# Performance work log

Hardware: AMD Instinct MI355X
Metric: run time of the kernel (lower is better)

## Reference

```python
import jax, jax.numpy as jnp
import numpy as np

MIN_NORM = 1e-15
BALL_EPS = 4e-3  # fp32 boundary eps used by PoincareBall.proj


def _artanh(x):
    x = jnp.clip(x, -1.0 + 1e-7, 1.0 - 1e-7)
    return 0.5 * (jnp.log1p(x) - jnp.log1p(-x))


def _norm(x):
    return jnp.maximum(jnp.linalg.norm(x, axis=-1, keepdims=True), MIN_NORM)


def mobius_matvec(m, x, c):
    sqrt_c = jnp.sqrt(c)
    x_norm = _norm(x)
    mx = x @ m  # [N, out]
    mx_norm = _norm(mx)
    res_c = jnp.tanh(mx_norm / x_norm * _artanh(sqrt_c * x_norm)) * mx / (mx_norm * sqrt_c)
    cond = jnp.all(mx == 0, axis=-1, keepdims=True)
    return jnp.where(cond, jnp.zeros((), dtype=x.dtype), res_c)


def expmap0(u, c):
    sqrt_c = jnp.sqrt(c)
    u_norm = _norm(u)
    return jnp.tanh(sqrt_c * u_norm) * u / (sqrt_c * u_norm)


def logmap0(p, c):
    sqrt_c = jnp.sqrt(c)
    p_norm = _norm(p)
    return _artanh(sqrt_c * p_norm) * p / (sqrt_c * p_norm)


def proj(x, c):
    norm = _norm(x)
    maxnorm = (1.0 - BALL_EPS) / jnp.sqrt(c)
    return jnp.where(norm > maxnorm, x / norm * maxnorm, x)


def mobius_add(x, y, c):
    x2 = jnp.sum(x * x, axis=-1, keepdims=True)
    y2 = jnp.sum(y * y, axis=-1, keepdims=True)
    xy = jnp.sum(x * y, axis=-1, keepdims=True)
    num = (1.0 + 2.0 * c * xy + c * y2) * x + (1.0 - c * x2) * y
    denom = 1.0 + 2.0 * c * xy + c * c * x2 * y2
    return num / jnp.maximum(denom, MIN_NORM)


def setup_inputs() -> dict:
    key = jax.random.key(0)
    N, E, IN, OUT = 50000, 800000, 256, 64
    ks = jax.random.split(key, 6)
    x = jax.random.normal(ks[0], (N, IN), dtype=jnp.float32) * 0.1
    weight = jax.random.normal(ks[1], (IN, OUT), dtype=jnp.float32) / np.sqrt(IN)
    bias = jax.random.normal(ks[2], (OUT,), dtype=jnp.float32) * 0.01
    vals = jax.random.uniform(ks[3], (E,), dtype=jnp.float32) / 16.0  # ~normalized adj
    row = jax.random.randint(ks[4], (E,), 0, N, dtype=jnp.int32)
    col = jax.random.randint(ks[5], (E,), 0, N, dtype=jnp.int32)
    c = jnp.asarray(1.0, dtype=jnp.float32)
    return {"x": x, "weight": weight, "bias": bias, "vals": vals, "c": c, "row": row, "col": col}


def reference(x, weight, bias, vals, c, row, col):
    N = x.shape[0]
    out = mobius_matvec(weight, x, c)
    # proj_tan0 is identity on the Poincare ball
    hyp_bias = proj(expmap0(bias[None, :], c), c)
    out = mobius_add(out, hyp_bias, c)
    out = logmap0(out, c)
    # sparse.mm(adj, out): gather neighbor rows, weight by edge vals, scatter-add
    out = jax.ops.segment_sum(vals[:, None] * out[col], row, num_segments=N)
    out = proj(expmap0(out, c), c)
    return out
```

## Files before the change

kernel.cpp:

```cpp
#include <hip/hip_runtime.h>
#include <math.h>

#define MIN_NORM 1e-15f
#define BALL_EPS 4e-3f

typedef __attribute__((ext_vector_type(8))) short bf16x8;
typedef __attribute__((ext_vector_type(4))) float f32x4;

__device__ __forceinline__ short f2bf(float f) {
  unsigned u = __builtin_bit_cast(unsigned, f);
  u = u + 0x7FFFu + ((u >> 16) & 1u);
  return (short)(u >> 16);
}
__device__ __forceinline__ float bf2f(unsigned short us) {
  unsigned u = ((unsigned)us) << 16;
  return __builtin_bit_cast(float, u);
}

__device__ __forceinline__ float wsum(float v) {
#pragma unroll
  for (int off = 32; off; off >>= 1) v += __shfl_xor(v, off, 64);
  return v;
}

__device__ __forceinline__ float artanh_clip(float z) {
  z = fminf(fmaxf(z, -1.0f + 1e-7f), 1.0f - 1e-7f);
  return 0.5f * (log1pf(z) - log1pf(-z));
}

__global__ __launch_bounds__(256) void k1_hyp_hist(
    const float* __restrict__ x, const float* __restrict__ W,
    const float* __restrict__ bias, const float* __restrict__ cptr,
    unsigned short* __restrict__ h, int N,
    const int* __restrict__ row, int* __restrict__ cnt, int E, int G1) {
  if ((int)blockIdx.x >= G1) {
    const int nb = gridDim.x - G1;
    for (int i = (blockIdx.x - G1) * 256 + threadIdx.x; i < E; i += nb * 256)
      atomicAdd(&cnt[row[i]], 1);
    return;
  }
  const int lane = threadIdx.x & 63;
  const int wid = threadIdx.x >> 6;
  const int m = lane & 15;
  const int g = lane >> 4;
  const float c = *cptr;
  const float sc = sqrtf(c);
  const float maxnorm = (1.0f - BALL_EPS) / sc;

  bf16x8 b[8][4];
#pragma unroll
  for (int kk = 0; kk < 8; ++kk)
#pragma unroll
    for (int t = 0; t < 4; ++t) {
      const float* wp = &W[(kk * 32 + g * 8) * 64 + t * 16 + m];
      bf16x8 bb;
#pragma unroll
      for (int j = 0; j < 8; ++j) bb[j] = f2bf(wp[j * 64]);
      b[kk][t] = bb;
    }

  float bv[4], bsq = 0.f;
#pragma unroll
  for (int t = 0; t < 4; ++t) { bv[t] = bias[t * 16 + m]; bsq += bv[t] * bv[t]; }
#pragma unroll
  for (int o = 1; o < 16; o <<= 1) bsq += __shfl_xor(bsq, o, 64);
  float bnorm = fmaxf(sqrtf(bsq), MIN_NORM);
  float tb = tanhf(sc * bnorm);
  float bfac = tb / (sc * bnorm);
  float hbn = fmaxf(tb / sc, MIN_NORM);
  float pfac = (hbn > maxnorm) ? (maxnorm / hbn) : 1.0f;
  float hbv[4], y2 = 0.f;
#pragma unroll
  for (int t = 0; t < 4; ++t) { hbv[t] = bv[t] * bfac * pfac; y2 += hbv[t] * hbv[t]; }
#pragma unroll
  for (int o = 1; o < 16; o <<= 1) y2 += __shfl_xor(y2, o, 64);

  const int nb16 = (N + 15) >> 4;
  const int wstep = G1 * 4;
  for (int rb = blockIdx.x * 4 + wid; rb < nb16; rb += wstep) {
    int arow = rb * 16 + m;
    if (arow >= N) arow = N - 1;
    const float* xp = &x[(size_t)arow * 256 + g * 8];

    bf16x8 a[8];
    float x2p = 0.f;
#pragma unroll
    for (int kk = 0; kk < 8; ++kk) {
      float4 v0 = *(const float4*)(xp + kk * 32);
      float4 v1 = *(const float4*)(xp + kk * 32 + 4);
      x2p += v0.x * v0.x + v0.y * v0.y + v0.z * v0.z + v0.w * v0.w +
             v1.x * v1.x + v1.y * v1.y + v1.z * v1.z + v1.w * v1.w;
      bf16x8 aa;
      aa[0] = f2bf(v0.x); aa[1] = f2bf(v0.y); aa[2] = f2bf(v0.z); aa[3] = f2bf(v0.w);
      aa[4] = f2bf(v1.x); aa[5] = f2bf(v1.y); aa[6] = f2bf(v1.z); aa[7] = f2bf(v1.w);
      a[kk] = aa;
    }
    float x2f = x2p;
    x2f += __shfl_xor(x2f, 16, 64);
    x2f += __shfl_xor(x2f, 32, 64);

    f32x4 acc[4];
#pragma unroll
    for (int t = 0; t < 4; ++t) { acc[t][0] = 0.f; acc[t][1] = 0.f; acc[t][2] = 0.f; acc[t][3] = 0.f; }
#pragma unroll
    for (int kk = 0; kk < 8; ++kk)
#pragma unroll
      for (int t = 0; t < 4; ++t)
        acc[t] = __builtin_amdgcn_mfma_f32_16x16x32_bf16(a[kk], b[kk][t], acc[t], 0, 0, 0);

    float x2r[4];
#pragma unroll
    for (int j = 0; j < 4; ++j) x2r[j] = __shfl(x2f, g * 4 + j, 64);

#pragma unroll
    for (int j = 0; j < 4; ++j) {
      float m0 = acc[0][j], m1 = acc[1][j], m2 = acc[2][j], m3 = acc[3][j];
      float msq = m0 * m0 + m1 * m1 + m2 * m2 + m3 * m3;
      int z = (m0 == 0.f) && (m1 == 0.f) && (m2 == 0.f) && (m3 == 0.f);
#pragma unroll
      for (int o = 1; o < 16; o <<= 1) {
        msq += __shfl_xor(msq, o, 64);
        z &= __shfl_xor(z, o, 64);
      }
      float mx_norm = fmaxf(sqrtf(msq), MIN_NORM);
      float x_norm = fmaxf(sqrtf(x2r[j]), MIN_NORM);
      float art = artanh_clip(sc * x_norm);
      float tt = tanhf(mx_norm / x_norm * art);
      float fac = z ? 0.f : (tt / (mx_norm * sc));
      float r0 = m0 * fac, r1 = m1 * fac, r2 = m2 * fac, r3 = m3 * fac;

      float x2m = r0 * r0 + r1 * r1 + r2 * r2 + r3 * r3;
      float xy = r0 * hbv[0] + r1 * hbv[1] + r2 * hbv[2] + r3 * hbv[3];
#pragma unroll
      for (int o = 1; o < 16; o <<= 1) {
        x2m += __shfl_xor(x2m, o, 64);
        xy += __shfl_xor(xy, o, 64);
      }
      float k2 = 1.f + 2.f * c * xy;
      float ca = k2 + c * y2;
      float cb = 1.f - c * x2m;
      float inv = 1.f / fmaxf(k2 + c * c * x2m * y2, MIN_NORM);
      float a0 = (ca * r0 + cb * hbv[0]) * inv;
      float a1 = (ca * r1 + cb * hbv[1]) * inv;
      float a2 = (ca * r2 + cb * hbv[2]) * inv;
      float a3 = (ca * r3 + cb * hbv[3]) * inv;

      float psq = a0 * a0 + a1 * a1 + a2 * a2 + a3 * a3;
#pragma unroll
      for (int o = 1; o < 16; o <<= 1) psq += __shfl_xor(psq, o, 64);
      float p_norm = fmaxf(sqrtf(psq), MIN_NORM);
      float art2 = artanh_clip(sc * p_norm);
      float fac2 = art2 / (sc * p_norm);

      int orow = rb * 16 + g * 4 + j;
      if (orow < N) {
        unsigned short* hp = &h[(size_t)orow * 64 + m];
        hp[0]  = (unsigned short)f2bf(a0 * fac2);
        hp[16] = (unsigned short)f2bf(a1 * fac2);
        hp[32] = (unsigned short)f2bf(a2 * fac2);
        hp[48] = (unsigned short)f2bf(a3 * fac2);
      }
    }
  }
}

__global__ __launch_bounds__(1024) void scan_a(const int* __restrict__ cnt,
                                               int* __restrict__ rowptr,
                                               int* __restrict__ blksum, int N) {
  __shared__ int wsums[16];
  int gid = blockIdx.x * 1024 + threadIdx.x;
  int lane = threadIdx.x & 63, w = threadIdx.x >> 6;
  int v = (gid < N) ? cnt[gid] : 0;
  int s = v;
#pragma unroll
  for (int d = 1; d < 64; d <<= 1) { int t = __shfl_up(s, d, 64); if (lane >= d) s += t; }
  if (lane == 63) wsums[w] = s;
  __syncthreads();
  if (w == 0 && lane < 16) {
    int ss = wsums[lane];
#pragma unroll
    for (int d = 1; d < 16; d <<= 1) { int u = __shfl_up(ss, d, 64); if (lane >= d) ss += u; }
    wsums[lane] = ss;
  }
  __syncthreads();
  if (w > 0) s += wsums[w - 1];
  if (gid < N) rowptr[1 + gid] = s;
  if (threadIdx.x == 1023) blksum[blockIdx.x] = s;
}

__global__ __launch_bounds__(1024) void scan_c(int* __restrict__ rowptr,
                                               const int* __restrict__ blksum,
                                               int N, int nblk) {
  __shared__ int s_off;
  if (threadIdx.x < 64) {
    int acc = 0;
    for (int bidx = threadIdx.x; bidx < (int)blockIdx.x; bidx += 64) acc += blksum[bidx];
#pragma unroll
    for (int off = 32; off; off >>= 1) acc += __shfl_xor(acc, off, 64);
    if (threadIdx.x == 0) s_off = acc;
  }
  __syncthreads();
  int gid = blockIdx.x * 1024 + threadIdx.x;
  if (gid == 0) rowptr[0] = 0;
  if (gid < N) rowptr[1 + gid] += s_off;
}

__global__ __launch_bounds__(256) void scatter_kernel(
    const int* __restrict__ row, const int* __restrict__ col,
    const float* __restrict__ vals, int* __restrict__ rowptr,
    int2* __restrict__ pairs, int E) {
  int i = blockIdx.x * blockDim.x + threadIdx.x;
  if (i < E) {
    int r = row[i];
    int pos = atomicAdd(&rowptr[r], 1);
    pairs[pos] = make_int2(col[i], __builtin_bit_cast(int, vals[i]));
  }
}

__global__ __launch_bounds__(256) void segsum_kernel(
    const unsigned short* __restrict__ h, const int* __restrict__ rowptr,
    const int2* __restrict__ pairs, const float* __restrict__ cptr,
    float* __restrict__ out, int N) {
  const int lane = threadIdx.x & 63;
  const int wid = threadIdx.x >> 6;
  const int sw = lane >> 4;
  const int q = lane & 15;
  int r = blockIdx.x * 4 + wid;
  if (r >= N) return;
  const float c = *cptr;
  const float sc = sqrtf(c);
  const float maxnorm = (1.0f - BALL_EPS) / sc;
  int st = (r > 0) ? rowptr[r - 1] : 0;
  int en = rowptr[r];
  st = __builtin_amdgcn_readfirstlane(st);
  en = __builtin_amdgcn_readfirstlane(en);

  float a0 = 0.f, a1 = 0.f, a2 = 0.f, a3 = 0.f;
#pragma unroll 2
  for (int i = st + sw; i < en; i += 4) {
    int2 pv = pairs[i];
    float vv = __builtin_bit_cast(float, pv.y);
    ushort4 hv = *(const ushort4*)&h[(size_t)pv.x * 64 + q * 4];
    a0 = fmaf(vv, bf2f(hv.x), a0);
    a1 = fmaf(vv, bf2f(hv.y), a1);
    a2 = fmaf(vv, bf2f(hv.z), a2);
    a3 = fmaf(vv, bf2f(hv.w), a3);
  }
  a0 += __shfl_xor(a0, 32, 64); a1 += __shfl_xor(a1, 32, 64);
  a2 += __shfl_xor(a2, 32, 64); a3 += __shfl_xor(a3, 32, 64);
  a0 += __shfl_xor(a0, 16, 64); a1 += __shfl_xor(a1, 16, 64);
  a2 += __shfl_xor(a2, 16, 64); a3 += __shfl_xor(a3, 16, 64);

  float sq = a0 * a0 + a1 * a1 + a2 * a2 + a3 * a3;
#pragma unroll
  for (int o = 1; o < 16; o <<= 1) sq += __shfl_xor(sq, o, 64);
  float un = fmaxf(sqrtf(sq), MIN_NORM);
  float th = tanhf(sc * un);
  float fac = th / (sc * un);
  float p0 = a0 * fac, p1 = a1 * fac, p2 = a2 * fac, p3 = a3 * fac;
  float psq = p0 * p0 + p1 * p1 + p2 * p2 + p3 * p3;
#pragma unroll
  for (int o = 1; o < 16; o <<= 1) psq += __shfl_xor(psq, o, 64);
  float pn = fmaxf(sqrtf(psq), MIN_NORM);
  if (pn > maxnorm) {
    float pf = maxnorm / pn;
    p0 *= pf; p1 *= pf; p2 *= pf; p3 *= pf;
  }
  if (sw == 0)
    *(float4*)&out[(size_t)r * 64 + q * 4] = make_float4(p0, p1, p2, p3);
}

__global__ __launch_bounds__(256) void edge_kernel(
    const unsigned short* __restrict__ h, const float* __restrict__ vals,
    const int* __restrict__ row, const int* __restrict__ col,
    float* __restrict__ out, int E) {
  const int lane = threadIdx.x & 63;
  const int wid0 = (blockIdx.x * blockDim.x + threadIdx.x) >> 6;
  const int nw = (gridDim.x * blockDim.x) >> 6;
  for (int e = wid0; e < E; e += nw) {
    int eu = __builtin_amdgcn_readfirstlane(e);
    float v = vals[eu];
    int r = row[eu];
    int cl = col[eu];
    atomicAdd(&out[(size_t)r * 64 + lane], v * bf2f(h[(size_t)cl * 64 + lane]));
  }
}

__global__ __launch_bounds__(256) void final_kernel(
    float* __restrict__ out, const float* __restrict__ cptr, int N) {
  const int lane = threadIdx.x & 63;
  const int wid0 = (blockIdx.x * blockDim.x + threadIdx.x) >> 6;
  const int nw = (gridDim.x * blockDim.x) >> 6;
  const float c = *cptr;
  const float sc = sqrtf(c);
  const float maxnorm = (1.0f - BALL_EPS) / sc;
  for (int r = wid0; r < N; r += nw) {
    float u = out[(size_t)r * 64 + lane];
    float un = fmaxf(sqrtf(wsum(u * u)), MIN_NORM);
    float th = tanhf(sc * un);
    float p = th * u / (sc * un);
    float pn = fmaxf(sqrtf(wsum(p * p)), MIN_NORM);
    if (pn > maxnorm) p = p / pn * maxnorm;
    out[(size_t)r * 64 + lane] = p;
  }
}

static inline size_t align256(size_t x) { return (x + 255) & ~(size_t)255; }

extern "C" void kernel_launch(void* const* d_in, const int* in_sizes, int n_in,
                              void* d_out, int out_size, void* d_ws, size_t ws_size,
                              hipStream_t stream) {
  const float* x = (const float*)d_in[0];
  const float* W = (const float*)d_in[1];
  const float* bias = (const float*)d_in[2];
  const float* vals = (const float*)d_in[3];
  const float* cptr = (const float*)d_in[4];
  const int* row = (const int*)d_in[5];
  const int* col = (const int*)d_in[6];
  float* out = (float*)d_out;

  const int OUT = in_sizes[2];
  const int IN = in_sizes[1] / OUT;
  const int N = in_sizes[0] / IN;
  const int E = in_sizes[3];

  char* ws = (char*)d_ws;
  size_t o_h = 0;
  size_t o_rowptr = align256(o_h + (size_t)N * 64 * 2);
  size_t o_blk = align256(o_rowptr + (size_t)(N + 1) * 4);
  size_t o_cnt = align256(o_blk + 1024 * 4);
  size_t o_pairs = align256(o_cnt + (size_t)N * 4);
  size_t needed = o_pairs + (size_t)E * 8;

  unsigned short* h = (unsigned short*)(ws + o_h);

  const int nb16 = (N + 15) / 16;
  const int G1 = (nb16 + 7) / 8;

  if (needed <= ws_size) {
    int* rowptr = (int*)(ws + o_rowptr);
    int* blksum = (int*)(ws + o_blk);
    int* cnt = (int*)(ws + o_cnt);
    int2* pairs = (int2*)(ws + o_pairs);

    const int nblk = (N + 1023) / 1024;
    const int eb = (E + 255) / 256;
    const int HB = 256;

    hipMemsetAsync(cnt, 0, (size_t)N * 4, stream);
    k1_hyp_hist<<<G1 + HB, 256, 0, stream>>>(x, W, bias, cptr, h, N, row, cnt, E, G1);
    scan_a<<<nblk, 1024, 0, stream>>>(cnt, rowptr, blksum, N);
    scan_c<<<nblk, 1024, 0, stream>>>(rowptr, blksum, N, nblk);
    scatter_kernel<<<eb, 256, 0, stream>>>(row, col, vals, rowptr, pairs, E);
    segsum_kernel<<<(N + 3) / 4, 256, 0, stream>>>(h, rowptr, pairs, cptr, out, N);
  } else {
    k1_hyp_hist<<<G1, 256, 0, stream>>>(x, W, bias, cptr, h, N, row, (int*)nullptr, 0, G1);
    hipMemsetAsync(d_out, 0, (size_t)out_size * sizeof(float), stream);
    edge_kernel<<<2048, 256, 0, stream>>>(h, vals, row, col, out, E);
    final_kernel<<<1024, 256, 0, stream>>>(out, cptr, N);
  }
}
```

Before: 228.6 us.

## Split GEMM and hyperbolic epilogue into separate kernels via fp32 workspace

Unfuses the first kernel. The MFMA GEMM now writes raw fp32 mx rows and per-row squared norms to workspace, and a new lightweight kernel reads them back with vectorized float4 loads to apply the mobius/logmap epilogue and write bf16 h. The aim is to shorten the GEMM kernel's critical path, lower its register pressure, and give coalesced ushort4 stores instead of strided 2-byte stores. The cost is an extra launch and an extra round trip of N*64*4 bytes through memory. The mx buffer is reused to hold the CSR pairs, which adds a size condition on the fast path.

```diff
diff --git a/kernel.cpp b/kernel.cpp
--- a/kernel.cpp
+++ b/kernel.cpp
@@ -28,10 +28,9 @@
   return 0.5f * (log1pf(z) - log1pf(-z));
 }
 
-__global__ __launch_bounds__(256) void k1_hyp_hist(
+__global__ __launch_bounds__(256) void k1_gemm_hist(
     const float* __restrict__ x, const float* __restrict__ W,
-    const float* __restrict__ bias, const float* __restrict__ cptr,
-    unsigned short* __restrict__ h, int N,
+    float* __restrict__ mx_ws, float* __restrict__ x2_ws, int N,
     const int* __restrict__ row, int* __restrict__ cnt, int E, int G1) {
   if ((int)blockIdx.x >= G1) {
     const int nb = gridDim.x - G1;
@@ -43,9 +42,6 @@
   const int wid = threadIdx.x >> 6;
   const int m = lane & 15;
   const int g = lane >> 4;
-  const float c = *cptr;
-  const float sc = sqrtf(c);
-  const float maxnorm = (1.0f - BALL_EPS) / sc;
 
   bf16x8 b[8][4];
 #pragma unroll
@@ -58,22 +54,6 @@
       for (int j = 0; j < 8; ++j) bb[j] = f2bf(wp[j * 64]);
       b[kk][t] = bb;
     }
-
-  float bv[4], bsq = 0.f;
-#pragma unroll
-  for (int t = 0; t < 4; ++t) { bv[t] = bias[t * 16 + m]; bsq += bv[t] * bv[t]; }
-#pragma unroll
-  for (int o = 1; o < 16; o <<= 1) bsq += __shfl_xor(bsq, o, 64);
-  float bnorm = fmaxf(sqrtf(bsq), MIN_NORM);
-  float tb = tanhf(sc * bnorm);
-  float bfac = tb / (sc * bnorm);
-  float hbn = fmaxf(tb / sc, MIN_NORM);
-  float pfac = (hbn > maxnorm) ? (maxnorm / hbn) : 1.0f;
-  float hbv[4], y2 = 0.f;
-#pragma unroll
-  for (int t = 0; t < 4; ++t) { hbv[t] = bv[t] * bfac * pfac; y2 += hbv[t] * hbv[t]; }
-#pragma unroll
-  for (int o = 1; o < 16; o <<= 1) y2 += __shfl_xor(y2, o, 64);
 
   const int nb16 = (N + 15) >> 4;
   const int wstep = G1 * 4;
@@ -108,60 +88,95 @@
       for (int t = 0; t < 4; ++t)
         acc[t] = __builtin_amdgcn_mfma_f32_16x16x32_bf16(a[kk], b[kk][t], acc[t], 0, 0, 0);
 
-    float x2r[4];
-#pragma unroll
-    for (int j = 0; j < 4; ++j) x2r[j] = __shfl(x2f, g * 4 + j, 64);
-
 #pragma unroll
     for (int j = 0; j < 4; ++j) {
-      float m0 = acc[0][j], m1 = acc[1][j], m2 = acc[2][j], m3 = acc[3][j];
-      float msq = m0 * m0 + m1 * m1 + m2 * m2 + m3 * m3;
-      int z = (m0 == 0.f) && (m1 == 0.f) && (m2 == 0.f) && (m3 == 0.f);
-#pragma unroll
-      for (int o = 1; o < 16; o <<= 1) {
-        msq += __shfl_xor(msq, o, 64);
-        z &= __shfl_xor(z, o, 64);
-      }
-      float mx_norm = fmaxf(sqrtf(msq), MIN_NORM);
-      float x_norm = fmaxf(sqrtf(x2r[j]), MIN_NORM);
-      float art = artanh_clip(sc * x_norm);
-      float tt = tanhf(mx_norm / x_norm * art);
-      float fac = z ? 0.f : (tt / (mx_norm * sc));
-      float r0 = m0 * fac, r1 = m1 * fac, r2 = m2 * fac, r3 = m3 * fac;
-
-      float x2m = r0 * r0 + r1 * r1 + r2 * r2 + r3 * r3;
-      float xy = r0 * hbv[0] + r1 * hbv[1] + r2 * hbv[2] + r3 * hbv[3];
-#pragma unroll
-      for (int o = 1; o < 16; o <<= 1) {
-        x2m += __shfl_xor(x2m, o, 64);
-        xy += __shfl_xor(xy, o, 64);
-      }
-      float k2 = 1.f + 2.f * c * xy;
-      float ca = k2 + c * y2;
-      float cb = 1.f - c * x2m;
-      float inv = 1.f / fmaxf(k2 + c * c * x2m * y2, MIN_NORM);
-      float a0 = (ca * r0 + cb * hbv[0]) * inv;
-      float a1 = (ca * r1 + cb * hbv[1]) * inv;
-      float a2 = (ca * r2 + cb * hbv[2]) * inv;
-      float a3 = (ca * r3 + cb * hbv[3]) * inv;
-
-      float psq = a0 * a0 + a1 * a1 + a2 * a2 + a3 * a3;
-#pragma unroll
-      for (int o = 1; o < 16; o <<= 1) psq += __shfl_xor(psq, o, 64);
-      float p_norm = fmaxf(sqrtf(psq), MIN_NORM);
-      float art2 = artanh_clip(sc * p_norm);
-      float fac2 = art2 / (sc * p_norm);
-
       int orow = rb * 16 + g * 4 + j;
       if (orow < N) {
-        unsigned short* hp = &h[(size_t)orow * 64 + m];
-        hp[0]  = (unsigned short)f2bf(a0 * fac2);
-        hp[16] = (unsigned short)f2bf(a1 * fac2);
-        hp[32] = (unsigned short)f2bf(a2 * fac2);
-        hp[48] = (unsigned short)f2bf(a3 * fac2);
+        float* mp = &mx_ws[(size_t)orow * 64 + m];
+#pragma unroll
+        for (int t = 0; t < 4; ++t) mp[t * 16] = acc[t][j];
       }
     }
-  }
+    if (g == 0 && rb * 16 + m < N) x2_ws[rb * 16 + m] = x2f;
+  }
+}
+
+__global__ __launch_bounds__(256) void k1b_hyp(
+    const float* __restrict__ mx_ws, const float* __restrict__ x2_ws,
+    const float* __restrict__ bias, const float* __restrict__ cptr,
+    unsigned short* __restrict__ h, int N) {
+  const int lane = threadIdx.x & 63;
+  const int wid = threadIdx.x >> 6;
+  const int sub = lane >> 4;
+  const int q = lane & 15;
+  const float c = *cptr;
+  const float sc = sqrtf(c);
+  const float maxnorm = (1.0f - BALL_EPS) / sc;
+
+  float4 bv = *(const float4*)&bias[q * 4];
+  float bsq = bv.x * bv.x + bv.y * bv.y + bv.z * bv.z + bv.w * bv.w;
+#pragma unroll
+  for (int o = 1; o < 16; o <<= 1) bsq += __shfl_xor(bsq, o, 64);
+  float bnorm = fmaxf(sqrtf(bsq), MIN_NORM);
+  float tb = tanhf(sc * bnorm);
+  float bfac = tb / (sc * bnorm);
+  float hbn = fmaxf(tb / sc, MIN_NORM);
+  float pfac = (hbn > maxnorm) ? (maxnorm / hbn) : 1.0f;
+  float hb0 = bv.x * bfac * pfac, hb1 = bv.y * bfac * pfac;
+  float hb2 = bv.z * bfac * pfac, hb3 = bv.w * bfac * pfac;
+  float y2 = hb0 * hb0 + hb1 * hb1 + hb2 * hb2 + hb3 * hb3;
+#pragma unroll
+  for (int o = 1; o < 16; o <<= 1) y2 += __shfl_xor(y2, o, 64);
+
+  const int r = (blockIdx.x * 4 + wid) * 4 + sub;
+  if (r >= N) return;
+
+  float4 mv = *(const float4*)&mx_ws[(size_t)r * 64 + q * 4];
+  float x2v = x2_ws[r];
+
+  float msq = mv.x * mv.x + mv.y * mv.y + mv.z * mv.z + mv.w * mv.w;
+  int z = (mv.x == 0.f) && (mv.y == 0.f) && (mv.z == 0.f) && (mv.w == 0.f);
+#pragma unroll
+  for (int o = 1; o < 16; o <<= 1) {
+    msq += __shfl_xor(msq, o, 64);
+    z &= __shfl_xor(z, o, 64);
+  }
+  float mx_norm = fmaxf(sqrtf(msq), MIN_NORM);
+  float x_norm = fmaxf(sqrtf(x2v), MIN_NORM);
+  float art = artanh_clip(sc * x_norm);
+  float tt = tanhf(mx_norm / x_norm * art);
+  float fac = z ? 0.f : (tt / (mx_norm * sc));
+  float r0 = mv.x * fac, r1 = mv.y * fac, r2 = mv.z * fac, r3 = mv.w * fac;
+
+  float x2m = r0 * r0 + r1 * r1 + r2 * r2 + r3 * r3;
+  float xy = r0 * hb0 + r1 * hb1 + r2 * hb2 + r3 * hb3;
+#pragma unroll
+  for (int o = 1; o < 16; o <<= 1) {
+    x2m += __shfl_xor(x2m, o, 64);
+    xy += __shfl_xor(xy, o, 64);
+  }
+  float k2 = 1.f + 2.f * c * xy;
+  float ca = k2 + c * y2;
+  float cb = 1.f - c * x2m;
+  float inv = 1.f / fmaxf(k2 + c * c * x2m * y2, MIN_NORM);
+  float a0 = (ca * r0 + cb * hb0) * inv;
+  float a1 = (ca * r1 + cb * hb1) * inv;
+  float a2 = (ca * r2 + cb * hb2) * inv;
+  float a3 = (ca * r3 + cb * hb3) * inv;
+
+  float psq = a0 * a0 + a1 * a1 + a2 * a2 + a3 * a3;
+#pragma unroll
+  for (int o = 1; o < 16; o <<= 1) psq += __shfl_xor(psq, o, 64);
+  float p_norm = fmaxf(sqrtf(psq), MIN_NORM);
+  float art2 = artanh_clip(sc * p_norm);
+  float fac2 = art2 / (sc * p_norm);
+
+  ushort4 hv;
+  hv.x = (unsigned short)f2bf(a0 * fac2);
+  hv.y = (unsigned short)f2bf(a1 * fac2);
+  hv.z = (unsigned short)f2bf(a2 * fac2);
+  hv.w = (unsigned short)f2bf(a3 * fac2);
+  *(ushort4*)&h[(size_t)r * 64 + q * 4] = hv;
 }
 
 __global__ __launch_bounds__(1024) void scan_a(const int* __restrict__ cnt,
@@ -325,36 +340,43 @@
   const int E = in_sizes[3];
 
   char* ws = (char*)d_ws;
-  size_t o_h = 0;
-  size_t o_rowptr = align256(o_h + (size_t)N * 64 * 2);
+  size_t o_mx = 0;
+  size_t o_h = align256(o_mx + (size_t)N * 64 * 4);
+  size_t o_x2 = align256(o_h + (size_t)N * 64 * 2);
+  size_t o_rowptr = align256(o_x2 + (size_t)N * 4);
   size_t o_blk = align256(o_rowptr + (size_t)(N + 1) * 4);
   size_t o_cnt = align256(o_blk + 1024 * 4);
-  size_t o_pairs = align256(o_cnt + (size_t)N * 4);
-  size_t needed = o_pairs + (size_t)E * 8;
-
+  size_t needed = o_cnt + (size_t)N * 4;
+  bool pairs_fit = (size_t)E * 8 <= o_h;
+
+  float* mx_ws = (float*)(ws + o_mx);
   unsigned short* h = (unsigned short*)(ws + o_h);
+  float* x2_ws = (float*)(ws + o_x2);
 
   const int nb16 = (N + 15) / 16;
   const int G1 = (nb16 + 7) / 8;
-
-  if (needed <= ws_size) {
+  const int HB = 256;
+  const int k1b_blocks = (N + 15) / 16;
+
+  if (needed <= ws_size && pairs_fit) {
     int* rowptr = (int*)(ws + o_rowptr);
     int* blksum = (int*)(ws + o_blk);
     int* cnt = (int*)(ws + o_cnt);
-    int2* pairs = (int2*)(ws + o_pairs);
+    int2* pairs = (int2*)(ws + o_mx);
 
     const int nblk = (N + 1023) / 1024;
     const int eb = (E + 255) / 256;
-    const int HB = 256;
 
     hipMemsetAsync(cnt, 0, (size_t)N * 4, stream);
-    k1_hyp_hist<<<G1 + HB, 256, 0, stream>>>(x, W, bias, cptr, h, N, row, cnt, E, G1);
+    k1_gemm_hist<<<G1 + HB, 256, 0, stream>>>(x, W, mx_ws, x2_ws, N, row, cnt, E, G1);
+    k1b_hyp<<<k1b_blocks, 256, 0, stream>>>(mx_ws, x2_ws, bias, cptr, h, N);
     scan_a<<<nblk, 1024, 0, stream>>>(cnt, rowptr, blksum, N);
     scan_c<<<nblk, 1024, 0, stream>>>(rowptr, blksum, N, nblk);
     scatter_kernel<<<eb, 256, 0, stream>>>(row, col, vals, rowptr, pairs, E);
     segsum_kernel<<<(N + 3) / 4, 256, 0, stream>>>(h, rowptr, pairs, cptr, out, N);
   } else {
-    k1_hyp_hist<<<G1, 256, 0, stream>>>(x, W, bias, cptr, h, N, row, (int*)nullptr, 0, G1);
+    k1_gemm_hist<<<G1, 256, 0, stream>>>(x, W, mx_ws, x2_ws, N, row, (int*)nullptr, 0, G1);
+    k1b_hyp<<<k1b_blocks, 256, 0, stream>>>(mx_ws, x2_ws, bias, cptr, h, N);
     hipMemsetAsync(d_out, 0, (size_t)out_size * sizeof(float), stream);
     edge_kernel<<<2048, 256, 0, stream>>>(h, vals, row, col, out, E);
     final_kernel<<<1024, 256, 0, stream>>>(out, cptr, N);
```

After: 227.3 us. No clear change (-0.6%).
